# Performance work log

Hardware: AMD Instinct MI355X
Metric: run time of the kernel (lower is better)

The kernel has to match this reference:

```python
import jax, jax.numpy as jnp
import numpy as np

INPUT_DIM, LATENT_DIM, HIDDEN_DIM, BATCH = 1024, 128, 1024, 32768


def setup_inputs() -> dict:
    key = jax.random.key(0)
    ks = jax.random.split(key, 12)
    s = 0.02
    x = (jax.random.uniform(ks[0], (BATCH, INPUT_DIM)) < 0.5).astype(jnp.float32)  # binary data
    eps = jax.random.normal(ks[1], (BATCH, LATENT_DIM), dtype=jnp.float32)
    return {
        "x": x,
        "eps": eps,
        "We1": jax.random.normal(ks[2], (INPUT_DIM, HIDDEN_DIM)) * s,
        "be1": jnp.zeros((HIDDEN_DIM,), jnp.float32),
        "Wmu": jax.random.normal(ks[3], (HIDDEN_DIM, LATENT_DIM)) * s,
        "bmu": jnp.zeros((LATENT_DIM,), jnp.float32),
        "Wls": jax.random.normal(ks[4], (HIDDEN_DIM, LATENT_DIM)) * s,
        "bls": jnp.zeros((LATENT_DIM,), jnp.float32),
        "Wd1": jax.random.normal(ks[5], (LATENT_DIM, HIDDEN_DIM)) * s,
        "bd1": jnp.zeros((HIDDEN_DIM,), jnp.float32),
        "Wd2": jax.random.normal(ks[6], (HIDDEN_DIM, INPUT_DIM)) * s,
        "bd2": jnp.zeros((INPUT_DIM,), jnp.float32),
    }


def reference(x, eps, We1, be1, Wmu, bmu, Wls, bls, Wd1, bd1, Wd2, bd2):
    # Encoder: one hidden ReLU layer, mu / logsigma heads
    h = jax.nn.relu(x @ We1 + be1)                      # [B, H]
    mu = h @ Wmu + bmu                                  # [B, L]
    logsigma = h @ Wls + bls                            # [B, L]
    # Reparameterization: z = sigma * eps + mu (vectorized diag(exp(logsigma)) @ eps)
    z = mu + jnp.exp(logsigma) * eps                    # [B, L]
    # Decoder: one hidden ReLU layer, sigmoid Bernoulli params
    hd = jax.nn.relu(z @ Wd1 + bd1)                     # [B, H]
    theta = jax.nn.sigmoid(hd @ Wd2 + bd2)              # [B, D]
    # Bernoulli log-likelihood: sum_j log(theta^x * (1-theta)^(1-x))
    log_px = jnp.sum(x * jnp.log(theta) + (1.0 - x) * jnp.log1p(-theta), axis=-1)  # [B]
    # KL(q||N(0,I)) = 0.5 * sum(sigma^2 + mu^2 - log(sigma^2) - 1)
    kl = 0.5 * jnp.sum(jnp.exp(2.0 * logsigma) + mu * mu - 2.0 * logsigma - 1.0, axis=-1)  # [B]
    return log_px - kl                                  # elbo_mc [B]
```

## Files before the change

kernel.cpp:

```cpp
#include <hip/hip_runtime.h>
#include <cstdint>
#include <cstddef>


typedef __bf16 bf16x8 __attribute__((ext_vector_type(8)));
typedef float f32x4 __attribute__((ext_vector_type(4)));

__device__ __forceinline__ unsigned short f32_to_bf16(float f) {
  unsigned int u = __float_as_uint(f);
  u += 0x7fffu + ((u >> 16) & 1u);
  return (unsigned short)(u >> 16);
}

struct TransJob { const float* in; unsigned short* out; int K, N, blkEnd; };

__global__ void prep_k(TransJob j0, TransJob j1, TransJob j2, TransJob j3,
                       TransJob j4, const float* __restrict__ x,
                       unsigned short* __restrict__ xbf, int n4) {
  int bid = blockIdx.x;
  int tid = threadIdx.y * 32 + threadIdx.x;
  if (bid >= 2432) {
    int base = (bid - 2432) * 256 + tid;
    int stride = 2048 * 256;
#pragma unroll
    for (int it = 0; it < 16; ++it) {
      int i = base + it * stride;
      float4 v = reinterpret_cast<const float4*>(x)[i];
      ushort4 o = make_ushort4(f32_to_bf16(v.x), f32_to_bf16(v.y),
                               f32_to_bf16(v.z), f32_to_bf16(v.w));
      reinterpret_cast<ushort4*>(xbf)[i] = o;
    }
    return;
  }
  __shared__ float tile[32][33];
  TransJob j; int base;
  if (bid < j0.blkEnd)      { j = j0; base = 0; }
  else if (bid < j1.blkEnd) { j = j1; base = j0.blkEnd; }
  else if (bid < j2.blkEnd) { j = j2; base = j1.blkEnd; }
  else if (bid < j3.blkEnd) { j = j3; base = j2.blkEnd; }
  else                      { j = j4; base = j3.blkEnd; }
  int local = bid - base;
  int gxN = j.N >> 5;
  int n0 = (local % gxN) * 32, k0 = (local / gxN) * 32;
  int tx = threadIdx.x, ty = threadIdx.y;
#pragma unroll
  for (int r = 0; r < 32; r += 8)
    tile[ty + r][tx] = j.in[(size_t)(k0 + ty + r) * j.N + n0 + tx];
  __syncthreads();
#pragma unroll
  for (int r = 0; r < 32; r += 8)
    j.out[(size_t)(n0 + ty + r) * j.K + k0 + tx] = f32_to_bf16(tile[tx][ty + r]);
}

__device__ __forceinline__ void gl_lds16(const unsigned short* g, unsigned short* l) {
  __builtin_amdgcn_global_load_lds(
      (__attribute__((address_space(1))) void*)g,
      (__attribute__((address_space(3))) void*)l, 16, 0, 0);
}

template <int EPI>
__global__ __launch_bounds__(256) void gemm_bt(
    const unsigned short* __restrict__ A, const unsigned short* __restrict__ BT,
    int gx, int N, int K,
    const float* __restrict__ bias0,
    unsigned short* __restrict__ outb, float* __restrict__ outf,
    const unsigned short* __restrict__ xbf) {
  __shared__ __align__(16) unsigned short As[128 * 64];
  __shared__ __align__(16) unsigned short Bs[128 * 64];

  const int tid = threadIdx.x;
  const int lane = tid & 63;
  const int wave = tid >> 6;
  const int wr = wave >> 1, wc = wave & 1;
  const int bid = blockIdx.x;
  const int xcd = bid & 7;
  const int t8 = bid >> 3;
  const int m0 = (xcd + 8 * (t8 / gx)) * 128;
  const int n0 = (t8 % gx) * 128;
  const int lm = lane & 15, lq = lane >> 4;

  const unsigned short* agp[4];
  const unsigned short* bgp[4];
#pragma unroll
  for (int r = 0; r < 4; ++r) {
    int c = tid + 256 * r;
    int row = c >> 3, q = (c & 7) ^ (row & 7);
    agp[r] = A + (size_t)(m0 + row) * K + q * 8;
    bgp[r] = BT + (size_t)(n0 + row) * K + q * 8;
  }
  const int sw = lm & 7;

  f32x4 acc[4][4] = {};

  for (int kt = 0; kt < K; kt += 64) {
#pragma unroll
    for (int r = 0; r < 4; ++r) {
      gl_lds16(agp[r] + kt, As + (tid + 256 * r) * 8);
      gl_lds16(bgp[r] + kt, Bs + (tid + 256 * r) * 8);
    }
    __syncthreads();

#pragma unroll
    for (int s = 0; s < 2; ++s) {
      const int so = ((s << 2) | lq) ^ sw;
      bf16x8 af[4], bfr[4];
#pragma unroll
      for (int i = 0; i < 4; ++i)
        af[i] = *reinterpret_cast<const bf16x8*>(As + (wr * 64 + i * 16 + lm) * 64 + so * 8);
#pragma unroll
      for (int j = 0; j < 4; ++j)
        bfr[j] = *reinterpret_cast<const bf16x8*>(Bs + (wc * 64 + j * 16 + lm) * 64 + so * 8);
#pragma unroll
      for (int i = 0; i < 4; ++i)
#pragma unroll
        for (int j = 0; j < 4; ++j)
          acc[i][j] = __builtin_amdgcn_mfma_f32_16x16x32_bf16(af[i], bfr[j], acc[i][j], 0, 0, 0);
    }
    __syncthreads();
  }

  if (EPI == 0) {
#pragma unroll
    for (int i = 0; i < 4; ++i)
#pragma unroll
      for (int j = 0; j < 4; ++j) {
        int col = n0 + wc * 64 + j * 16 + lm;
        float bias = bias0[col];
#pragma unroll
        for (int r = 0; r < 4; ++r) {
          int row = m0 + wr * 64 + i * 16 + lq * 4 + r;
          float v = acc[i][j][r] + bias;
          v = fmaxf(v, 0.f);
          outb[(size_t)row * N + col] = f32_to_bf16(v);
        }
      }
  } else {
#pragma unroll
    for (int i = 0; i < 4; ++i) {
      float rs[4] = {0.f, 0.f, 0.f, 0.f};
#pragma unroll
      for (int j = 0; j < 4; ++j) {
        int col = n0 + wc * 64 + j * 16 + lm;
        float bias = bias0[col];
#pragma unroll
        for (int r = 0; r < 4; ++r) {
          int row = m0 + wr * 64 + i * 16 + lq * 4 + r;
          float l = acc[i][j][r] + bias;
          unsigned short xb = xbf[(size_t)row * N + col];
          float t = xb ? -l : l;
          float sp = fmaxf(t, 0.f) + __logf(1.f + __expf(-fabsf(t)));
          rs[r] -= sp;
        }
      }
#pragma unroll
      for (int off = 1; off < 16; off <<= 1)
#pragma unroll
        for (int r = 0; r < 4; ++r) rs[r] += __shfl_xor(rs[r], off, 64);
      if (lm == 0) {
#pragma unroll
        for (int r = 0; r < 4; ++r)
          atomicAdd(&outf[m0 + wr * 64 + i * 16 + lq * 4 + r], rs[r]);
      }
    }
  }
}

__global__ __launch_bounds__(256) void gemm2_zkl(
    const unsigned short* __restrict__ A,
    const unsigned short* __restrict__ BT,
    int K,
    const float* __restrict__ bmu, const float* __restrict__ bls,
    const float* __restrict__ eps,
    unsigned short* __restrict__ z,
    float* __restrict__ out) {
  __shared__ __align__(16) unsigned short As[64 * 64];
  __shared__ __align__(16) unsigned short Bs[256 * 64];

  const int tid = threadIdx.x;
  const int lane = tid & 63;
  const int wave = tid >> 6;
  const int m0 = blockIdx.x * 64;
  const int lm = lane & 15, lq = lane >> 4;

  const unsigned short* agp[2];
  const unsigned short* bgp[8];
#pragma unroll
  for (int r = 0; r < 2; ++r) {
    int c = tid + 256 * r;
    int row = c >> 3, q = (c & 7) ^ (row & 7);
    agp[r] = A + (size_t)(m0 + row) * K + q * 8;
  }
#pragma unroll
  for (int r = 0; r < 8; ++r) {
    int c = tid + 256 * r;
    int row = c >> 3, q = (c & 7) ^ (row & 7);
    bgp[r] = BT + (size_t)row * K + q * 8;
  }
  const int sw = lm & 7;

  f32x4 acc[16] = {};

  for (int kt = 0; kt < K; kt += 64) {
#pragma unroll
    for (int r = 0; r < 2; ++r) gl_lds16(agp[r] + kt, As + (tid + 256 * r) * 8);
#pragma unroll
    for (int r = 0; r < 8; ++r) gl_lds16(bgp[r] + kt, Bs + (tid + 256 * r) * 8);
    __syncthreads();

#pragma unroll
    for (int s = 0; s < 2; ++s) {
      const int so = ((s << 2) | lq) ^ sw;
      bf16x8 af = *reinterpret_cast<const bf16x8*>(As + (wave * 16 + lm) * 64 + so * 8);
#pragma unroll
      for (int j = 0; j < 16; ++j) {
        bf16x8 b = *reinterpret_cast<const bf16x8*>(Bs + (j * 16 + lm) * 64 + so * 8);
        acc[j] = __builtin_amdgcn_mfma_f32_16x16x32_bf16(af, b, acc[j], 0, 0, 0);
      }
    }
    __syncthreads();
  }

  float kl[4] = {0.f, 0.f, 0.f, 0.f};
#pragma unroll
  for (int j = 0; j < 8; ++j) {
    int dim = j * 16 + lm;
    float bm = bmu[dim], bl = bls[dim];
#pragma unroll
    for (int r = 0; r < 4; ++r) {
      int row = m0 + wave * 16 + lq * 4 + r;
      float mu = acc[j][r] + bm;
      float ls = acc[j + 8][r] + bl;
      float e = eps[(size_t)row * 128 + dim];
      z[(size_t)row * 128 + dim] = f32_to_bf16(fmaf(__expf(ls), e, mu));
      kl[r] += 0.5f * (__expf(2.f * ls) + mu * mu - 2.f * ls - 1.f);
    }
  }
#pragma unroll
  for (int off = 1; off < 16; off <<= 1)
#pragma unroll
    for (int r = 0; r < 4; ++r) kl[r] += __shfl_xor(kl[r], off, 64);
  if (lm == 0) {
#pragma unroll
    for (int r = 0; r < 4; ++r)
      out[m0 + wave * 16 + lq * 4 + r] = -kl[r];
  }
}

extern "C" void kernel_launch(void* const* d_in, const int* in_sizes, int n_in,
                              void* d_out, int out_size, void* d_ws, size_t ws_size,
                              hipStream_t stream) {
  const float* x   = (const float*)d_in[0];
  const float* eps = (const float*)d_in[1];
  const float* We1 = (const float*)d_in[2];
  const float* be1 = (const float*)d_in[3];
  const float* Wmu = (const float*)d_in[4];
  const float* bmu = (const float*)d_in[5];
  const float* Wls = (const float*)d_in[6];
  const float* bls = (const float*)d_in[7];
  const float* Wd1 = (const float*)d_in[8];
  const float* bd1 = (const float*)d_in[9];
  const float* Wd2 = (const float*)d_in[10];
  const float* bd2 = (const float*)d_in[11];
  float* out = (float*)d_out;

  const int B = 32768, D = 1024, H = 1024, L = 128;

  char* ws = (char*)d_ws;
  size_t off = 0;
  auto alloc = [&](size_t bytes) {
    void* p = ws + off;
    off += (bytes + 255) & ~(size_t)255;
    return p;
  };
  unsigned short* xbf  = (unsigned short*)alloc((size_t)B * D * 2);
  unsigned short* w1t  = (unsigned short*)alloc((size_t)H * D * 2);
  unsigned short* w2t  = (unsigned short*)alloc((size_t)256 * H * 2);
  unsigned short* wd1t = (unsigned short*)alloc((size_t)H * L * 2);
  unsigned short* wd2t = (unsigned short*)alloc((size_t)D * H * 2);
  unsigned short* h    = (unsigned short*)alloc((size_t)B * H * 2);
  unsigned short* z    = (unsigned short*)alloc((size_t)B * L * 2);
  unsigned short* hd   = h;

  TransJob j0{We1, w1t, D, H, 1024};
  TransJob j1{Wmu, w2t, H, L, 1152};
  TransJob j2{Wls, w2t + 128 * H, H, L, 1280};
  TransJob j3{Wd1, wd1t, L, H, 1408};
  TransJob j4{Wd2, wd2t, H, D, 2432};
  prep_k<<<4480, dim3(32, 8), 0, stream>>>(j0, j1, j2, j3, j4, x, xbf, B * D / 4);

  gemm_bt<0><<<8 * 256, 256, 0, stream>>>(
      xbf, w1t, 8, H, D, be1, h, nullptr, nullptr);
  gemm2_zkl<<<B / 64, 256, 0, stream>>>(h, w2t, H, bmu, bls, eps, z, out);
  gemm_bt<0><<<8 * 256, 256, 0, stream>>>(
      z, wd1t, 8, H, L, bd1, hd, nullptr, nullptr);
  gemm_bt<2><<<8 * 256, 256, 0, stream>>>(
      hd, wd2t, 8, D, H, bd2, nullptr, out, xbf);

  (void)in_sizes; (void)n_in; (void)out_size; (void)ws_size;
}
```

Before: 483.2 us.

## Fuse decoder first layer into mu/logsigma GEMM kernel via LDS-resident z

The z@Wd1+bd1 ReLU GEMM is folded into the mu/logsigma/KL kernel. The reparameterized z tile is written in bf16 to swizzled shared memory instead of global memory. The same block then streams Wd1 in 128-column chunks to produce hd directly. This drops one kernel launch and the global write and re-read of z, but the hd stores are narrow 2-byte scattered writes and each block now reloads all of Wd1.

```diff
diff --git a/kernel.cpp b/kernel.cpp
--- a/kernel.cpp
+++ b/kernel.cpp
@@ -165,22 +165,27 @@
   }
 }
 
-__global__ __launch_bounds__(256) void gemm2_zkl(
+__global__ __launch_bounds__(256) void gemm23_zkl(
     const unsigned short* __restrict__ A,
     const unsigned short* __restrict__ BT,
-    int K,
+    const unsigned short* __restrict__ WD1,
     const float* __restrict__ bmu, const float* __restrict__ bls,
+    const float* __restrict__ bd1,
     const float* __restrict__ eps,
-    unsigned short* __restrict__ z,
+    unsigned short* __restrict__ hd,
     float* __restrict__ out) {
-  __shared__ __align__(16) unsigned short As[64 * 64];
-  __shared__ __align__(16) unsigned short Bs[256 * 64];
+  __shared__ __align__(16) unsigned short lds[24576];
+  unsigned short* As = lds;
+  unsigned short* Bs = lds + 4096;
+  unsigned short* zs = lds;
+  unsigned short* Ws = lds + 8192;
 
   const int tid = threadIdx.x;
   const int lane = tid & 63;
   const int wave = tid >> 6;
   const int m0 = blockIdx.x * 64;
   const int lm = lane & 15, lq = lane >> 4;
+  const int K = 1024;
 
   const unsigned short* agp[2];
   const unsigned short* bgp[8];
@@ -225,13 +230,16 @@
   for (int j = 0; j < 8; ++j) {
     int dim = j * 16 + lm;
     float bm = bmu[dim], bl = bls[dim];
+    int chunk = dim >> 3;
 #pragma unroll
     for (int r = 0; r < 4; ++r) {
-      int row = m0 + wave * 16 + lq * 4 + r;
+      int lr = wave * 16 + lq * 4 + r;
       float mu = acc[j][r] + bm;
       float ls = acc[j + 8][r] + bl;
-      float e = eps[(size_t)row * 128 + dim];
-      z[(size_t)row * 128 + dim] = f32_to_bf16(fmaf(__expf(ls), e, mu));
+      float e = eps[(size_t)(m0 + lr) * 128 + dim];
+      float zz = fmaf(__expf(ls), e, mu);
+      int slot = chunk ^ (lr & 15);
+      zs[lr * 128 + slot * 8 + (dim & 7)] = f32_to_bf16(zz);
       kl[r] += 0.5f * (__expf(2.f * ls) + mu * mu - 2.f * ls - 1.f);
     }
   }
@@ -243,6 +251,57 @@
 #pragma unroll
     for (int r = 0; r < 4; ++r)
       out[m0 + wave * 16 + lq * 4 + r] = -kl[r];
+  }
+
+  int wrow[8], wq[8];
+#pragma unroll
+  for (int r = 0; r < 8; ++r) {
+    int c = tid + 256 * r;
+    wrow[r] = c >> 4;
+    wq[r] = (c & 15) ^ (wrow[r] & 15);
+  }
+
+  for (int cc = 0; cc < 8; ++cc) {
+#pragma unroll
+    for (int r = 0; r < 8; ++r)
+      gl_lds16(WD1 + (size_t)(cc * 128 + wrow[r]) * 128 + wq[r] * 8,
+               Ws + (tid + 256 * r) * 8);
+    __syncthreads();
+
+    f32x4 acc2[4][2] = {};
+#pragma unroll
+    for (int s = 0; s < 4; ++s) {
+      const int c = (s << 2) | lq;
+      const int so = c ^ lm;
+      bf16x8 af[4];
+#pragma unroll
+      for (int it = 0; it < 4; ++it)
+        af[it] = *reinterpret_cast<const bf16x8*>(zs + (it * 16 + lm) * 128 + so * 8);
+#pragma unroll
+      for (int jt = 0; jt < 2; ++jt) {
+        bf16x8 b = *reinterpret_cast<const bf16x8*>(
+            Ws + (wave * 32 + jt * 16 + lm) * 128 + so * 8);
+#pragma unroll
+        for (int it = 0; it < 4; ++it)
+          acc2[it][jt] = __builtin_amdgcn_mfma_f32_16x16x32_bf16(af[it], b, acc2[it][jt], 0, 0, 0);
+      }
+    }
+    __syncthreads();
+
+#pragma unroll
+    for (int jt = 0; jt < 2; ++jt) {
+      int col = cc * 128 + wave * 32 + jt * 16 + lm;
+      float bias = bd1[col];
+#pragma unroll
+      for (int it = 0; it < 4; ++it)
+#pragma unroll
+        for (int r = 0; r < 4; ++r) {
+          int row = m0 + it * 16 + lq * 4 + r;
+          float v = acc2[it][jt][r] + bias;
+          v = fmaxf(v, 0.f);
+          hd[(size_t)row * 1024 + col] = f32_to_bf16(v);
+        }
+    }
   }
 }
 
@@ -278,7 +337,6 @@
   unsigned short* wd1t = (unsigned short*)alloc((size_t)H * L * 2);
   unsigned short* wd2t = (unsigned short*)alloc((size_t)D * H * 2);
   unsigned short* h    = (unsigned short*)alloc((size_t)B * H * 2);
-  unsigned short* z    = (unsigned short*)alloc((size_t)B * L * 2);
   unsigned short* hd   = h;
 
   TransJob j0{We1, w1t, D, H, 1024};
@@ -290,9 +348,7 @@
 
   gemm_bt<0><<<8 * 256, 256, 0, stream>>>(
       xbf, w1t, 8, H, D, be1, h, nullptr, nullptr);
-  gemm2_zkl<<<B / 64, 256, 0, stream>>>(h, w2t, H, bmu, bls, eps, z, out);
-  gemm_bt<0><<<8 * 256, 256, 0, stream>>>(
-      z, wd1t, 8, H, L, bd1, hd, nullptr, nullptr);
+  gemm23_zkl<<<B / 64, 256, 0, stream>>>(h, w2t, wd1t, bmu, bls, bd1, eps, hd, out);
   gemm_bt<2><<<8 * 256, 256, 0, stream>>>(
       hd, wd2t, 8, D, H, bd2, nullptr, out, xbf);
 
```

After: 484.5 us. No clear change (+0.3%).
